# Optimization experiments

Measured on AMD Instinct MI355X. Metric: run time of the kernel, lower is better.

The kernel has to match this reference:

```python
import jax, jax.numpy as jnp
import numpy as np
from jax import lax

T_LOW, T_HIGH = 100.0, 200.0   # init kwargs of Canny
TG22 = 0.4142135623730951      # tan(22.5 deg), cv2's direction quantization constant
MAX_ITERS = 512                # safety cap on hysteresis fixed-point loop


def _shift(a, dy, dx):
    # neighbor value n[y, x] = a[y + dy, x + dx], zero outside
    H, W = a.shape
    p = jnp.pad(a, 1)
    return p[1 + dy:1 + dy + H, 1 + dx:1 + dx + W]


def _canny(x):
    B, C, H, W = x.shape
    # toRGB: ((x+1)/2*255).to(uint8)  (truncation; values are non-negative)
    img = jnp.clip(jnp.floor((x + 1.0) * 0.5 * 255.0), 0.0, 255.0)
    # original reshapes batch into one tall strip (B*H, W, C) before cv2.Canny
    img = img.transpose(0, 2, 3, 1).reshape(B * H, W, C)
    HH = B * H
    p = jnp.pad(img, ((1, 1), (1, 1), (0, 0)), mode='edge')  # replicate border like cv2

    def s(dy, dx):
        return p[1 + dy:1 + dy + HH, 1 + dx:1 + dx + W, :]

    # 3x3 Sobel per channel
    gx = (s(-1, 1) + 2.0 * s(0, 1) + s(1, 1)) - (s(-1, -1) + 2.0 * s(0, -1) + s(1, -1))
    gy = (s(1, -1) + 2.0 * s(1, 0) + s(1, 1)) - (s(-1, -1) + 2.0 * s(-1, 0) + s(-1, 1))
    mag_c = jnp.abs(gx) + jnp.abs(gy)  # L1 magnitude (cv2 default L2gradient=False)
    # multi-channel: take channel with max magnitude per pixel (cv2 behavior)
    idx = jnp.argmax(mag_c, axis=-1, keepdims=True)
    gx = jnp.take_along_axis(gx, idx, -1)[..., 0]
    gy = jnp.take_along_axis(gy, idx, -1)[..., 0]
    mag = jnp.take_along_axis(mag_c, idx, -1)[..., 0]

    # non-maximum suppression with 4 quantized directions
    ax_, ay_ = jnp.abs(gx), jnp.abs(gy)
    is_h = ay_ < TG22 * ax_          # gradient ~horizontal -> compare left/right
    is_v = ay_ * TG22 > ax_          # gradient ~vertical -> compare up/down
    same = (gx * gy) >= 0.0          # diagonal orientation by sign agreement
    n1 = jnp.where(is_h, _shift(mag, 0, -1),
         jnp.where(is_v, _shift(mag, -1, 0),
         jnp.where(same, _shift(mag, -1, -1), _shift(mag, -1, 1))))
    n2 = jnp.where(is_h, _shift(mag, 0, 1),
         jnp.where(is_v, _shift(mag, 1, 0),
         jnp.where(same, _shift(mag, 1, 1), _shift(mag, 1, -1))))
    keep = (mag > n1) & (mag >= n2)

    strong = keep & (mag > T_HIGH)
    weak = keep & (mag > T_LOW)

    # hysteresis: propagate strong labels through 8-connected weak pixels to fixed point
    def dilate(m):
        mf = m.astype(jnp.float32)
        return lax.reduce_window(mf, 0.0, lax.add, (3, 3), (1, 1), 'SAME') > 0.0

    def body(st):
        s0, _, it = st
        grown = (dilate(s0) & weak) | s0
        return grown, jnp.any(grown != s0), it + 1

    def cond(st):
        return st[1] & (st[2] < MAX_ITERS)

    strong, _, _ = lax.while_loop(cond, body, (strong, jnp.array(True), jnp.array(0)))

    edges = strong.reshape(B, H, W).astype(jnp.float32)        # {0,1} == cv2 {0,255}/255
    edges = jnp.broadcast_to(edges[:, None, :, :], (B, 3, H, W))
    return (edges - 0.5) / 0.5                                 # T.Normalize(0.5, 0.5)


def setup_inputs() -> dict:
    key = jax.random.key(0)
    x = jax.random.uniform(key, (16, 3, 512, 512), jnp.float32, -1.0, 1.0)
    return {"x": x}


def reference(x):
    return _canny(x)
```

## Files before the change

kernel.cpp:

```cpp
#include <hip/hip_runtime.h>
#include <stdint.h>

#define HH 8192
#define WW 512
#define WPR 8
#define TG22F 0.4142135623730951f
#define NROUND 8
#define NBLK 32


__device__ __forceinline__ float to_img(float v) {
    float t = floorf((v + 1.0f) * 0.5f * 255.0f);
    return fminf(fmaxf(t, 0.0f), 255.0f);
}

__device__ __forceinline__ int bsel(uint64_t w0, uint64_t w1, int idx) {
    return (idx < 8) ? (int)((w0 >> (idx * 8)) & 255)
                     : (int)((w1 >> ((idx - 8) * 8)) & 255);
}

__device__ __forceinline__ uint64_t runfill(uint64_t s, uint64_t w) {
    uint64_t sw = s & w;
    uint64_t up = ((sw + w) ^ w) & w;
    uint64_t rs = __brevll(sw);
    uint64_t rw = __brevll(w);
    uint64_t dn = __brevll(((rs + rw) ^ rw) & rw);
    return up | dn | sw;
}

__device__ __forceinline__ uint64_t shfl_up64(uint64_t v, int d) {
    int lo = __shfl_up((int)(uint32_t)v, d, 64);
    int hi = __shfl_up((int)(uint32_t)(v >> 32), d, 64);
    return ((uint64_t)(uint32_t)hi << 32) | (uint32_t)lo;
}
__device__ __forceinline__ uint64_t shfl_dn64(uint64_t v, int d) {
    int lo = __shfl_down((int)(uint32_t)v, d, 64);
    int hi = __shfl_down((int)(uint32_t)(v >> 32), d, 64);
    return ((uint64_t)(uint32_t)hi << 32) | (uint32_t)lo;
}

__device__ __forceinline__ uint64_t cload64(const unsigned long long* p) {
    return __hip_atomic_load((const unsigned long long*)p, __ATOMIC_RELAXED,
                             __HIP_MEMORY_SCOPE_AGENT);
}
__device__ __forceinline__ void cstore64(unsigned long long* p, uint64_t v) {
    __hip_atomic_store(p, (unsigned long long)v, __ATOMIC_RELAXED,
                       __HIP_MEMORY_SCOPE_AGENT);
}

__global__ void k_sobel(const float* __restrict__ in, uint16_t* __restrict__ packed) {
    __shared__ uint8_t simg[3 * 34 * 72];
    const int tid = threadIdx.x;
    const int row0 = (blockIdx.x >> 3) << 5;
    const int col0 = (blockIdx.x & 7) << 6;

    for (int i = tid; i < 1632; i += 256) {
        int c = i / 544;
        int rem = i - c * 544;
        int hr = rem >> 4;
        int q = rem & 15;
        int gy = row0 + hr - 1;
        gy = gy < 0 ? 0 : (gy >= HH ? HH - 1 : gy);
        int b = gy >> 9, h = gy & 511;
        const float4 v = *(const float4*)&in[((((b * 3 + c) << 9) + h) << 9) + col0 + (q << 2)];
        uint32_t pk = (uint32_t)(uint8_t)to_img(v.x)
                    | ((uint32_t)(uint8_t)to_img(v.y) << 8)
                    | ((uint32_t)(uint8_t)to_img(v.z) << 16)
                    | ((uint32_t)(uint8_t)to_img(v.w) << 24);
        *(uint32_t*)&simg[(c * 34 + hr) * 72 + 4 + (q << 2)] = pk;
    }
    for (int i = tid; i < 204; i += 256) {
        int c = i / 68;
        int rem = i - c * 68;
        int hr = rem >> 1;
        int side = rem & 1;
        int gy = row0 + hr - 1;
        gy = gy < 0 ? 0 : (gy >= HH ? HH - 1 : gy);
        int gc = side ? col0 + 64 : col0 - 1;
        gc = gc < 0 ? 0 : (gc >= WW ? WW - 1 : gc);
        int b = gy >> 9, h = gy & 511;
        float v = to_img(in[((((b * 3 + c) << 9) + h) << 9) + gc]);
        simg[(c * 34 + hr) * 72 + (side ? 68 : 3)] = (uint8_t)v;
    }
    __syncthreads();

    const int r = tid >> 3;
    const int c8 = (tid & 7) << 3;

    int bestMag[8], bgx[8], bgy[8];
    #pragma unroll
    for (int j = 0; j < 8; ++j) { bestMag[j] = -1; bgx[j] = 0; bgy[j] = 0; }

    #pragma unroll
    for (int c = 0; c < 3; ++c) {
        const uint8_t* base = &simg[(c * 34 + r) * 72 + c8];
        uint64_t w00 = *(const uint64_t*)(base);
        uint64_t w01 = *(const uint64_t*)(base + 8);
        uint64_t w10 = *(const uint64_t*)(base + 72);
        uint64_t w11 = *(const uint64_t*)(base + 80);
        uint64_t w20 = *(const uint64_t*)(base + 144);
        uint64_t w21 = *(const uint64_t*)(base + 152);
        int vs[10], t0[10], t2[10];
        #pragma unroll
        for (int i = 0; i < 10; ++i) {
            int a0 = bsel(w00, w01, 3 + i);
            int a1 = bsel(w10, w11, 3 + i);
            int a2 = bsel(w20, w21, 3 + i);
            vs[i] = a0 + 2 * a1 + a2;
            t0[i] = a0; t2[i] = a2;
        }
        #pragma unroll
        for (int j = 0; j < 8; ++j) {
            int gx = vs[j + 2] - vs[j];
            int gy = (t2[j] + 2 * t2[j + 1] + t2[j + 2]) - (t0[j] + 2 * t0[j + 1] + t0[j + 2]);
            int mg = abs(gx) + abs(gy);
            if (mg > bestMag[j]) { bestMag[j] = mg; bgx[j] = gx; bgy[j] = gy; }
        }
    }

    uint32_t res[4];
    #pragma unroll
    for (int jj = 0; jj < 4; ++jj) {
        uint32_t pair = 0;
        #pragma unroll
        for (int s = 0; s < 2; ++s) {
            int j = jj * 2 + s;
            float axf = (float)abs(bgx[j]);
            float ayf = (float)abs(bgy[j]);
            int dir;
            if (ayf < TG22F * axf)      dir = 0;
            else if (ayf * TG22F > axf) dir = 1;
            else                        dir = (bgx[j] * bgy[j] >= 0) ? 2 : 3;
            uint32_t val = (uint32_t)(bestMag[j] | (dir << 12));
            pair |= val << (s * 16);
        }
        res[jj] = pair;
    }
    int y = row0 + r;
    *(uint4*)&packed[y * WW + col0 + c8] = *(uint4*)res;
}

#define MEXT(lo, hi, idx) ((int)((((idx) < 4 ? ((lo) >> (16 * (idx))) \
                                             : ((hi) >> (16 * ((idx) - 4))))) & 0xFFF))

__global__ void k_nms(const uint16_t* __restrict__ packed,
                      unsigned long long* __restrict__ strongB,
                      unsigned long long* __restrict__ weakB,
                      int* __restrict__ flags) {
    if (blockIdx.x == 0 && threadIdx.x < 16) flags[threadIdx.x] = 0;
    const int lane = threadIdx.x & 63;
    const int w = threadIdx.x >> 6;
    const int y = (blockIdx.x << 2) + w;

    uint4 q = *(const uint4*)&packed[y * WW + (lane << 3)];
    uint64_t oLo = ((uint64_t)q.y << 32) | q.x;
    uint64_t oHi = ((uint64_t)q.w << 32) | q.z;
    uint64_t uLo = 0, uHi = 0, dLo = 0, dHi = 0;
    if (y > 0) {
        uint4 qu = *(const uint4*)&packed[(y - 1) * WW + (lane << 3)];
        uLo = ((uint64_t)qu.y << 32) | qu.x;
        uHi = ((uint64_t)qu.w << 32) | qu.z;
    }
    if (y < HH - 1) {
        uint4 qd = *(const uint4*)&packed[(y + 1) * WW + (lane << 3)];
        dLo = ((uint64_t)qd.y << 32) | qd.x;
        dHi = ((uint64_t)qd.w << 32) | qd.z;
    }

    int oL = __shfl_up((int)((oHi >> 48) & 0xFFF), 1, 64); if (lane == 0) oL = 0;
    int uL = __shfl_up((int)((uHi >> 48) & 0xFFF), 1, 64); if (lane == 0) uL = 0;
    int dL = __shfl_up((int)((dHi >> 48) & 0xFFF), 1, 64); if (lane == 0) dL = 0;
    int oR = __shfl_down((int)(oLo & 0xFFF), 1, 64); if (lane == 63) oR = 0;
    int uR = __shfl_down((int)(uLo & 0xFFF), 1, 64); if (lane == 63) uR = 0;
    int dR = __shfl_down((int)(dLo & 0xFFF), 1, 64); if (lane == 63) dR = 0;

    uint32_t sb = 0, wb = 0;
    #pragma unroll
    for (int i = 0; i < 8; ++i) {
        int raw = (int)(((i < 4 ? (oLo >> (16 * i)) : (oHi >> (16 * (i - 4))))) & 0xFFFF);
        int m = raw & 0xFFF;
        int dir = raw >> 12;
        int Om1 = (i == 0) ? oL : MEXT(oLo, oHi, (i == 0 ? 0 : i - 1));
        int Op1 = (i == 7) ? oR : MEXT(oLo, oHi, (i == 7 ? 7 : i + 1));
        int Ui  = MEXT(uLo, uHi, i);
        int Um1 = (i == 0) ? uL : MEXT(uLo, uHi, (i == 0 ? 0 : i - 1));
        int Up1 = (i == 7) ? uR : MEXT(uLo, uHi, (i == 7 ? 7 : i + 1));
        int Di  = MEXT(dLo, dHi, i);
        int Dm1 = (i == 0) ? dL : MEXT(dLo, dHi, (i == 0 ? 0 : i - 1));
        int Dp1 = (i == 7) ? dR : MEXT(dLo, dHi, (i == 7 ? 7 : i + 1));
        int n1 = (dir == 0) ? Om1 : (dir == 1) ? Ui : (dir == 2) ? Um1 : Up1;
        int n2 = (dir == 0) ? Op1 : (dir == 1) ? Di : (dir == 2) ? Dp1 : Dm1;
        bool keep = (m > n1) && (m >= n2);
        if (keep && m > 200) sb |= 1u << i;
        if (keep && m > 100) wb |= 1u << i;
    }

    const int src = (lane & 7) << 3;
    uint64_t wordS = 0, wordW = 0;
    #pragma unroll
    for (int i = 0; i < 8; ++i) {
        wordS |= (uint64_t)(uint32_t)__shfl((int)sb, src + i, 64) << (i * 8);
        wordW |= (uint64_t)(uint32_t)__shfl((int)wb, src + i, 64) << (i * 8);
    }
    if (lane < 8)       strongB[y * WPR + lane] = wordS;
    else if (lane < 16) weakB[y * WPR + (lane - 8)] = wordW;
}

__global__ void __launch_bounds__(256) k_hyst(
        const unsigned long long* __restrict__ weakB,
        unsigned long long* __restrict__ buf,
        int* __restrict__ flags)
{
    const int lane = threadIdx.x & 63;
    const int wave = (blockIdx.x << 2) + (threadIdx.x >> 6);
    const int base = ((wave << 6) + lane) * WPR;

    uint64_t own[8], wk[8];
    #pragma unroll
    for (int k = 0; k < 8; ++k) { wk[k] = weakB[base + k]; own[k] = buf[base + k]; }

    uint64_t hspu[8], hspd[8];
    #pragma unroll
    for (int k = 0; k < 8; ++k) { hspu[k] = 0; hspd[k] = 0; }

    auto load_halo = [&]() {
        uint64_t h[8];
        if (lane == 0 && wave > 0) {
            #pragma unroll
            for (int k = 0; k < 8; ++k) h[k] = cload64(&buf[base - WPR + k]);
            #pragma unroll
            for (int k = 0; k < 8; ++k) {
                uint64_t a = h[k] | (h[k] << 1) | (h[k] >> 1);
                if (k > 0) a |= h[k - 1] >> 63;
                if (k < 7) a |= h[k + 1] << 63;
                hspu[k] = a;
            }
        }
        if (lane == 63 && wave < 127) {
            #pragma unroll
            for (int k = 0; k < 8; ++k) h[k] = cload64(&buf[base + WPR + k]);
            #pragma unroll
            for (int k = 0; k < 8; ++k) {
                uint64_t a = h[k] | (h[k] << 1) | (h[k] >> 1);
                if (k > 0) a |= h[k - 1] >> 63;
                if (k < 7) a |= h[k + 1] << 63;
                hspd[k] = a;
            }
        }
    };
    load_halo();

    bool grewAny = false;
    for (int r = 0; r < NROUND; ++r) {
        bool grew = false;
        for (;;) {
            uint64_t sp[8];
            #pragma unroll
            for (int k = 0; k < 8; ++k) {
                uint64_t h = own[k] | (own[k] << 1) | (own[k] >> 1);
                if (k > 0) h |= own[k - 1] >> 63;
                if (k < 7) h |= own[k + 1] << 63;
                sp[k] = h;
            }
            uint64_t su[8], sd[8];
            #pragma unroll
            for (int k = 0; k < 8; ++k) {
                su[k] = shfl_up64(sp[k], 1);
                sd[k] = shfl_dn64(sp[k], 1);
            }
            if (lane == 0) {
                #pragma unroll
                for (int k = 0; k < 8; ++k) su[k] = hspu[k];
            }
            if (lane == 63) {
                #pragma unroll
                for (int k = 0; k < 8; ++k) sd[k] = hspd[k];
            }
            uint32_t ch = 0;
            #pragma unroll
            for (int k = 0; k < 8; ++k) {
                uint64_t acc = sp[k] | su[k] | sd[k];
                uint64_t nv = runfill(own[k] | (acc & wk[k]), wk[k]);
                ch |= (uint32_t)(nv != own[k]);
                own[k] = nv;
            }
            if (ch) grew = true;
            if (__ballot(ch ? 1 : 0) == 0ull) break;
        }
        grewAny |= grew;

        if (grew && lane == 0)
            __hip_atomic_store(&flags[r], 1, __ATOMIC_RELAXED, __HIP_MEMORY_SCOPE_AGENT);
        if (lane == 0 || lane == 63) {
            #pragma unroll
            for (int k = 0; k < 8; ++k) cstore64(&buf[base + k], own[k]);
        }
        __syncthreads();
        if (threadIdx.x == 0) {
            __hip_atomic_fetch_add(&flags[8 + r], 1, __ATOMIC_RELAXED, __HIP_MEMORY_SCOPE_AGENT);
            while (__hip_atomic_load(&flags[8 + r], __ATOMIC_RELAXED, __HIP_MEMORY_SCOPE_AGENT) < NBLK)
                __builtin_amdgcn_s_sleep(2);
        }
        __syncthreads();

        if (__hip_atomic_load(&flags[r], __ATOMIC_RELAXED, __HIP_MEMORY_SCOPE_AGENT) == 0)
            break;
        if (r + 1 < NROUND) load_halo();
    }

    if (__ballot(grewAny ? 1 : 0) != 0ull) {
        #pragma unroll
        for (int k = 0; k < 8; ++k) buf[base + k] = own[k];
    }
}

__global__ void k_out(const unsigned long long* __restrict__ result, float* __restrict__ out) {
    int t = blockIdx.x * blockDim.x + threadIdx.x;
    int b = t >> 16;
    int r = t & 65535;
    int h = r >> 7;
    int w = (r & 127) << 2;
    int y = (b << 9) + h;
    unsigned long long word = result[y * WPR + (w >> 6)];
    int sh = w & 63;
    float4 v;
    v.x = ((word >> (sh + 0)) & 1ull) ? 1.0f : -1.0f;
    v.y = ((word >> (sh + 1)) & 1ull) ? 1.0f : -1.0f;
    v.z = ((word >> (sh + 2)) & 1ull) ? 1.0f : -1.0f;
    v.w = ((word >> (sh + 3)) & 1ull) ? 1.0f : -1.0f;
    int base = (b * 3) << 18;
    int off = (h << 9) + w;
    *(float4*)&out[base + off] = v;
    *(float4*)&out[base + 262144 + off] = v;
    *(float4*)&out[base + 524288 + off] = v;
}

extern "C" void kernel_launch(void* const* d_in, const int* in_sizes, int n_in,
                              void* d_out, int out_size, void* d_ws, size_t ws_size,
                              hipStream_t stream) {
    const float* x = (const float*)d_in[0];
    float* out = (float*)d_out;
    char* ws = (char*)d_ws;

    uint16_t* packed          = (uint16_t*)(ws);
    unsigned long long* buf   = (unsigned long long*)(ws + 8388608);
    unsigned long long* weakB = (unsigned long long*)(ws + 8912896);
    int* flags                = (int*)(ws + 9437184);

    k_sobel<<<2048, 256, 0, stream>>>(x, packed);
    k_nms<<<2048, 256, 0, stream>>>(packed, buf, weakB, flags);
    k_hyst<<<NBLK, 256, 0, stream>>>(weakB, buf, flags);
    k_out<<<4096, 256, 0, stream>>>(buf, out);
}
```

Measured before the change: 122.9 us.

## Fuse NMS, hysteresis and output into one persistent kernel with grid barriers

Merges the NMS, hysteresis and output-expansion kernels into a single persistent kernel of 512 blocks. Two software grid barriers built on atomic counters separate the phases, and only the first 32 blocks run the hysteresis loop. Flag clearing moves into the Sobel kernel. The aim is to remove two kernel launches and their gaps, at the cost of idle blocks spinning during hysteresis and relying on all 512 blocks being co-resident.

```diff
diff --git a/kernel.cpp b/kernel.cpp
--- a/kernel.cpp
+++ b/kernel.cpp
@@ -7,6 +7,7 @@
 #define TG22F 0.4142135623730951f
 #define NROUND 8
 #define NBLK 32
+#define TBLK 512
 
 
 __device__ __forceinline__ float to_img(float v) {
@@ -48,11 +49,24 @@
                        __HIP_MEMORY_SCOPE_AGENT);
 }
 
-__global__ void k_sobel(const float* __restrict__ in, uint16_t* __restrict__ packed) {
+__device__ __forceinline__ void gbar(int* flags, int slot, int target) {
+    __syncthreads();
+    if (threadIdx.x == 0) {
+        __hip_atomic_fetch_add(&flags[slot], 1, __ATOMIC_RELAXED, __HIP_MEMORY_SCOPE_AGENT);
+        while (__hip_atomic_load(&flags[slot], __ATOMIC_RELAXED, __HIP_MEMORY_SCOPE_AGENT) < target)
+            __builtin_amdgcn_s_sleep(2);
+    }
+    __syncthreads();
+}
+
+__global__ void k_sobel(const float* __restrict__ in, uint16_t* __restrict__ packed,
+                        int* __restrict__ flags) {
     __shared__ uint8_t simg[3 * 34 * 72];
     const int tid = threadIdx.x;
     const int row0 = (blockIdx.x >> 3) << 5;
     const int col0 = (blockIdx.x & 7) << 6;
+
+    if (blockIdx.x == 0 && tid < 32) flags[tid] = 0;
 
     for (int i = tid; i < 1632; i += 256) {
         int c = i / 544;
@@ -143,15 +157,10 @@
 #define MEXT(lo, hi, idx) ((int)((((idx) < 4 ? ((lo) >> (16 * (idx))) \
                                              : ((hi) >> (16 * ((idx) - 4))))) & 0xFFF))
 
-__global__ void k_nms(const uint16_t* __restrict__ packed,
-                      unsigned long long* __restrict__ strongB,
-                      unsigned long long* __restrict__ weakB,
-                      int* __restrict__ flags) {
-    if (blockIdx.x == 0 && threadIdx.x < 16) flags[threadIdx.x] = 0;
-    const int lane = threadIdx.x & 63;
-    const int w = threadIdx.x >> 6;
-    const int y = (blockIdx.x << 2) + w;
-
+__device__ __forceinline__ void nms_row(int y, int lane,
+        const uint16_t* __restrict__ packed,
+        unsigned long long* __restrict__ strongB,
+        unsigned long long* __restrict__ weakB) {
     uint4 q = *(const uint4*)&packed[y * WW + (lane << 3)];
     uint64_t oLo = ((uint64_t)q.y << 32) | q.x;
     uint64_t oHi = ((uint64_t)q.w << 32) | q.z;
@@ -202,137 +211,159 @@
         wordS |= (uint64_t)(uint32_t)__shfl((int)sb, src + i, 64) << (i * 8);
         wordW |= (uint64_t)(uint32_t)__shfl((int)wb, src + i, 64) << (i * 8);
     }
-    if (lane < 8)       strongB[y * WPR + lane] = wordS;
-    else if (lane < 16) weakB[y * WPR + (lane - 8)] = wordW;
-}
-
-__global__ void __launch_bounds__(256) k_hyst(
-        const unsigned long long* __restrict__ weakB,
+    if (lane < 8)       cstore64(&strongB[y * WPR + lane], wordS);
+    else if (lane < 16) cstore64(&weakB[y * WPR + (lane - 8)], wordW);
+}
+
+__device__ __forceinline__ void out_row(int y, int lane,
+        const unsigned long long* __restrict__ buf, float* __restrict__ out) {
+    const int b = y >> 9, h = y & 511;
+    const int obase = ((b * 3) << 18) + (h << 9);
+    #pragma unroll
+    for (int i = 0; i < 2; ++i) {
+        int idx = lane + (i << 6);
+        uint64_t wv = cload64(&buf[y * WPR + (idx >> 4)]);
+        int x = idx << 2;
+        int sh = x & 63;
+        float4 v;
+        v.x = ((wv >> (sh + 0)) & 1ull) ? 1.0f : -1.0f;
+        v.y = ((wv >> (sh + 1)) & 1ull) ? 1.0f : -1.0f;
+        v.z = ((wv >> (sh + 2)) & 1ull) ? 1.0f : -1.0f;
+        v.w = ((wv >> (sh + 3)) & 1ull) ? 1.0f : -1.0f;
+        *(float4*)&out[obase + x] = v;
+        *(float4*)&out[obase + (1 << 18) + x] = v;
+        *(float4*)&out[obase + (2 << 18) + x] = v;
+    }
+}
+
+__global__ void __launch_bounds__(256) k_nho(
+        const uint16_t* __restrict__ packed,
         unsigned long long* __restrict__ buf,
-        int* __restrict__ flags)
+        unsigned long long* __restrict__ weakB,
+        int* __restrict__ flags,
+        float* __restrict__ out)
 {
     const int lane = threadIdx.x & 63;
-    const int wave = (blockIdx.x << 2) + (threadIdx.x >> 6);
-    const int base = ((wave << 6) + lane) * WPR;
-
-    uint64_t own[8], wk[8];
-    #pragma unroll
-    for (int k = 0; k < 8; ++k) { wk[k] = weakB[base + k]; own[k] = buf[base + k]; }
-
-    uint64_t hspu[8], hspd[8];
-    #pragma unroll
-    for (int k = 0; k < 8; ++k) { hspu[k] = 0; hspd[k] = 0; }
-
-    auto load_halo = [&]() {
-        uint64_t h[8];
-        if (lane == 0 && wave > 0) {
-            #pragma unroll
-            for (int k = 0; k < 8; ++k) h[k] = cload64(&buf[base - WPR + k]);
-            #pragma unroll
-            for (int k = 0; k < 8; ++k) {
-                uint64_t a = h[k] | (h[k] << 1) | (h[k] >> 1);
-                if (k > 0) a |= h[k - 1] >> 63;
-                if (k < 7) a |= h[k + 1] << 63;
-                hspu[k] = a;
-            }
-        }
-        if (lane == 63 && wave < 127) {
-            #pragma unroll
-            for (int k = 0; k < 8; ++k) h[k] = cload64(&buf[base + WPR + k]);
-            #pragma unroll
-            for (int k = 0; k < 8; ++k) {
-                uint64_t a = h[k] | (h[k] << 1) | (h[k] >> 1);
-                if (k > 0) a |= h[k - 1] >> 63;
-                if (k < 7) a |= h[k + 1] << 63;
-                hspd[k] = a;
-            }
-        }
-    };
-    load_halo();
-
-    bool grewAny = false;
-    for (int r = 0; r < NROUND; ++r) {
-        bool grew = false;
-        for (;;) {
-            uint64_t sp[8];
-            #pragma unroll
-            for (int k = 0; k < 8; ++k) {
-                uint64_t h = own[k] | (own[k] << 1) | (own[k] >> 1);
-                if (k > 0) h |= own[k - 1] >> 63;
-                if (k < 7) h |= own[k + 1] << 63;
-                sp[k] = h;
-            }
-            uint64_t su[8], sd[8];
-            #pragma unroll
-            for (int k = 0; k < 8; ++k) {
-                su[k] = shfl_up64(sp[k], 1);
-                sd[k] = shfl_dn64(sp[k], 1);
-            }
-            if (lane == 0) {
-                #pragma unroll
-                for (int k = 0; k < 8; ++k) su[k] = hspu[k];
-            }
-            if (lane == 63) {
-                #pragma unroll
-                for (int k = 0; k < 8; ++k) sd[k] = hspd[k];
-            }
-            uint32_t ch = 0;
-            #pragma unroll
-            for (int k = 0; k < 8; ++k) {
-                uint64_t acc = sp[k] | su[k] | sd[k];
-                uint64_t nv = runfill(own[k] | (acc & wk[k]), wk[k]);
-                ch |= (uint32_t)(nv != own[k]);
-                own[k] = nv;
-            }
-            if (ch) grew = true;
-            if (__ballot(ch ? 1 : 0) == 0ull) break;
-        }
-        grewAny |= grew;
-
-        if (grew && lane == 0)
-            __hip_atomic_store(&flags[r], 1, __ATOMIC_RELAXED, __HIP_MEMORY_SCOPE_AGENT);
-        if (lane == 0 || lane == 63) {
+    const int widx = threadIdx.x >> 6;
+    const int wv = (blockIdx.x << 2) + widx;
+
+    #pragma unroll
+    for (int r = 0; r < 4; ++r)
+        nms_row((wv << 2) + r, lane, packed, buf, weakB);
+
+    gbar(flags, 16, TBLK);
+
+    if (blockIdx.x < NBLK) {
+        const int wave = (blockIdx.x << 2) + widx;
+        const int base = ((wave << 6) + lane) * WPR;
+
+        uint64_t own[8], wk[8];
+        #pragma unroll
+        for (int k = 0; k < 8; ++k) {
+            wk[k]  = cload64(&weakB[base + k]);
+            own[k] = cload64(&buf[base + k]);
+        }
+
+        uint64_t hspu[8], hspd[8];
+        #pragma unroll
+        for (int k = 0; k < 8; ++k) { hspu[k] = 0; hspd[k] = 0; }
+
+        auto load_halo = [&]() {
+            uint64_t h[8];
+            if (lane == 0 && wave > 0) {
+                #pragma unroll
+                for (int k = 0; k < 8; ++k) h[k] = cload64(&buf[base - WPR + k]);
+                #pragma unroll
+                for (int k = 0; k < 8; ++k) {
+                    uint64_t a = h[k] | (h[k] << 1) | (h[k] >> 1);
+                    if (k > 0) a |= h[k - 1] >> 63;
+                    if (k < 7) a |= h[k + 1] << 63;
+                    hspu[k] = a;
+                }
+            }
+            if (lane == 63 && wave < 127) {
+                #pragma unroll
+                for (int k = 0; k < 8; ++k) h[k] = cload64(&buf[base + WPR + k]);
+                #pragma unroll
+                for (int k = 0; k < 8; ++k) {
+                    uint64_t a = h[k] | (h[k] << 1) | (h[k] >> 1);
+                    if (k > 0) a |= h[k - 1] >> 63;
+                    if (k < 7) a |= h[k + 1] << 63;
+                    hspd[k] = a;
+                }
+            }
+        };
+        load_halo();
+
+        bool grewAny = false;
+        for (int r = 0; r < NROUND; ++r) {
+            bool grew = false;
+            for (;;) {
+                uint64_t sp[8];
+                #pragma unroll
+                for (int k = 0; k < 8; ++k) {
+                    uint64_t h = own[k] | (own[k] << 1) | (own[k] >> 1);
+                    if (k > 0) h |= own[k - 1] >> 63;
+                    if (k < 7) h |= own[k + 1] << 63;
+                    sp[k] = h;
+                }
+                uint64_t su[8], sd[8];
+                #pragma unroll
+                for (int k = 0; k < 8; ++k) {
+                    su[k] = shfl_up64(sp[k], 1);
+                    sd[k] = shfl_dn64(sp[k], 1);
+                }
+                if (lane == 0) {
+                    #pragma unroll
+                    for (int k = 0; k < 8; ++k) su[k] = hspu[k];
+                }
+                if (lane == 63) {
+                    #pragma unroll
+                    for (int k = 0; k < 8; ++k) sd[k] = hspd[k];
+                }
+                uint32_t ch = 0;
+                #pragma unroll
+                for (int k = 0; k < 8; ++k) {
+                    uint64_t acc = sp[k] | su[k] | sd[k];
+                    uint64_t nv = runfill(own[k] | (acc & wk[k]), wk[k]);
+                    ch |= (uint32_t)(nv != own[k]);
+                    own[k] = nv;
+                }
+                if (ch) grew = true;
+                if (__ballot(ch ? 1 : 0) == 0ull) break;
+            }
+            grewAny |= grew;
+
+            if (grew && lane == 0)
+                __hip_atomic_store(&flags[r], 1, __ATOMIC_RELAXED, __HIP_MEMORY_SCOPE_AGENT);
+            if (lane == 0 || lane == 63) {
+                #pragma unroll
+                for (int k = 0; k < 8; ++k) cstore64(&buf[base + k], own[k]);
+            }
+            __syncthreads();
+            if (threadIdx.x == 0) {
+                __hip_atomic_fetch_add(&flags[8 + r], 1, __ATOMIC_RELAXED, __HIP_MEMORY_SCOPE_AGENT);
+                while (__hip_atomic_load(&flags[8 + r], __ATOMIC_RELAXED, __HIP_MEMORY_SCOPE_AGENT) < NBLK)
+                    __builtin_amdgcn_s_sleep(2);
+            }
+            __syncthreads();
+
+            if (__hip_atomic_load(&flags[r], __ATOMIC_RELAXED, __HIP_MEMORY_SCOPE_AGENT) == 0)
+                break;
+            if (r + 1 < NROUND) load_halo();
+        }
+
+        if (__ballot(grewAny ? 1 : 0) != 0ull) {
             #pragma unroll
             for (int k = 0; k < 8; ++k) cstore64(&buf[base + k], own[k]);
         }
-        __syncthreads();
-        if (threadIdx.x == 0) {
-            __hip_atomic_fetch_add(&flags[8 + r], 1, __ATOMIC_RELAXED, __HIP_MEMORY_SCOPE_AGENT);
-            while (__hip_atomic_load(&flags[8 + r], __ATOMIC_RELAXED, __HIP_MEMORY_SCOPE_AGENT) < NBLK)
-                __builtin_amdgcn_s_sleep(2);
-        }
-        __syncthreads();
-
-        if (__hip_atomic_load(&flags[r], __ATOMIC_RELAXED, __HIP_MEMORY_SCOPE_AGENT) == 0)
-            break;
-        if (r + 1 < NROUND) load_halo();
-    }
-
-    if (__ballot(grewAny ? 1 : 0) != 0ull) {
-        #pragma unroll
-        for (int k = 0; k < 8; ++k) buf[base + k] = own[k];
-    }
-}
-
-__global__ void k_out(const unsigned long long* __restrict__ result, float* __restrict__ out) {
-    int t = blockIdx.x * blockDim.x + threadIdx.x;
-    int b = t >> 16;
-    int r = t & 65535;
-    int h = r >> 7;
-    int w = (r & 127) << 2;
-    int y = (b << 9) + h;
-    unsigned long long word = result[y * WPR + (w >> 6)];
-    int sh = w & 63;
-    float4 v;
-    v.x = ((word >> (sh + 0)) & 1ull) ? 1.0f : -1.0f;
-    v.y = ((word >> (sh + 1)) & 1ull) ? 1.0f : -1.0f;
-    v.z = ((word >> (sh + 2)) & 1ull) ? 1.0f : -1.0f;
-    v.w = ((word >> (sh + 3)) & 1ull) ? 1.0f : -1.0f;
-    int base = (b * 3) << 18;
-    int off = (h << 9) + w;
-    *(float4*)&out[base + off] = v;
-    *(float4*)&out[base + 262144 + off] = v;
-    *(float4*)&out[base + 524288 + off] = v;
+    }
+
+    gbar(flags, 17, TBLK);
+
+    #pragma unroll
+    for (int r = 0; r < 4; ++r)
+        out_row((wv << 2) + r, lane, buf, out);
 }
 
 extern "C" void kernel_launch(void* const* d_in, const int* in_sizes, int n_in,
@@ -347,8 +378,6 @@
     unsigned long long* weakB = (unsigned long long*)(ws + 8912896);
     int* flags                = (int*)(ws + 9437184);
 
-    k_sobel<<<2048, 256, 0, stream>>>(x, packed);
-    k_nms<<<2048, 256, 0, stream>>>(packed, buf, weakB, flags);
-    k_hyst<<<NBLK, 256, 0, stream>>>(weakB, buf, flags);
-    k_out<<<4096, 256, 0, stream>>>(buf, out);
-}
+    k_sobel<<<2048, 256, 0, stream>>>(x, packed, flags);
+    k_nho<<<TBLK, 256, 0, stream>>>(packed, buf, weakB, flags, out);
+}
```

Result: slower. 150.6 us (+22.5%).

## Replace shared-memory tiled Sobel with per-wave row loads and lane shuffles

Applied to the files above, without the earlier changes.

The Sobel kernel no longer stages a 32x64 tile plus halo into shared memory. Each wavefront now handles one full image row, loading the three neighbouring rows directly from global memory and exchanging left/right halo pixels with lane shuffles. This removes the LDS staging, the __syncthreads barrier and the byte-extraction logic. In exchange every input row is read three times from global memory (relying on cache), and the launch geometry must match the new one-row-per-wave mapping.

```diff
diff --git a/kernel.cpp b/kernel.cpp
--- a/kernel.cpp
+++ b/kernel.cpp
@@ -12,11 +12,6 @@
 __device__ __forceinline__ float to_img(float v) {
     float t = floorf((v + 1.0f) * 0.5f * 255.0f);
     return fminf(fmaxf(t, 0.0f), 255.0f);
-}
-
-__device__ __forceinline__ int bsel(uint64_t w0, uint64_t w1, int idx) {
-    return (idx < 8) ? (int)((w0 >> (idx * 8)) & 255)
-                     : (int)((w1 >> ((idx - 8) * 8)) & 255);
 }
 
 __device__ __forceinline__ uint64_t runfill(uint64_t s, uint64_t w) {
@@ -48,44 +43,31 @@
                        __HIP_MEMORY_SCOPE_AGENT);
 }
 
+__device__ __forceinline__ void load_row10(const float* __restrict__ in,
+                                           int row, int c, int lane, int a[10]) {
+    const float* p = &in[(size_t)((((row >> 9) * 3 + c) << 9) + (row & 511)) << 9];
+    const int x0 = lane << 3;
+    float4 v0 = *(const float4*)&p[x0];
+    float4 v1 = *(const float4*)&p[x0 + 4];
+    a[1] = (int)(uint8_t)to_img(v0.x);
+    a[2] = (int)(uint8_t)to_img(v0.y);
+    a[3] = (int)(uint8_t)to_img(v0.z);
+    a[4] = (int)(uint8_t)to_img(v0.w);
+    a[5] = (int)(uint8_t)to_img(v1.x);
+    a[6] = (int)(uint8_t)to_img(v1.y);
+    a[7] = (int)(uint8_t)to_img(v1.z);
+    a[8] = (int)(uint8_t)to_img(v1.w);
+    int l = __shfl_up(a[8], 1, 64);
+    a[0] = (lane == 0) ? a[1] : l;
+    int r = __shfl_down(a[1], 1, 64);
+    a[9] = (lane == 63) ? a[8] : r;
+}
+
 __global__ void k_sobel(const float* __restrict__ in, uint16_t* __restrict__ packed) {
-    __shared__ uint8_t simg[3 * 34 * 72];
-    const int tid = threadIdx.x;
-    const int row0 = (blockIdx.x >> 3) << 5;
-    const int col0 = (blockIdx.x & 7) << 6;
-
-    for (int i = tid; i < 1632; i += 256) {
-        int c = i / 544;
-        int rem = i - c * 544;
-        int hr = rem >> 4;
-        int q = rem & 15;
-        int gy = row0 + hr - 1;
-        gy = gy < 0 ? 0 : (gy >= HH ? HH - 1 : gy);
-        int b = gy >> 9, h = gy & 511;
-        const float4 v = *(const float4*)&in[((((b * 3 + c) << 9) + h) << 9) + col0 + (q << 2)];
-        uint32_t pk = (uint32_t)(uint8_t)to_img(v.x)
-                    | ((uint32_t)(uint8_t)to_img(v.y) << 8)
-                    | ((uint32_t)(uint8_t)to_img(v.z) << 16)
-                    | ((uint32_t)(uint8_t)to_img(v.w) << 24);
-        *(uint32_t*)&simg[(c * 34 + hr) * 72 + 4 + (q << 2)] = pk;
-    }
-    for (int i = tid; i < 204; i += 256) {
-        int c = i / 68;
-        int rem = i - c * 68;
-        int hr = rem >> 1;
-        int side = rem & 1;
-        int gy = row0 + hr - 1;
-        gy = gy < 0 ? 0 : (gy >= HH ? HH - 1 : gy);
-        int gc = side ? col0 + 64 : col0 - 1;
-        gc = gc < 0 ? 0 : (gc >= WW ? WW - 1 : gc);
-        int b = gy >> 9, h = gy & 511;
-        float v = to_img(in[((((b * 3 + c) << 9) + h) << 9) + gc]);
-        simg[(c * 34 + hr) * 72 + (side ? 68 : 3)] = (uint8_t)v;
-    }
-    __syncthreads();
-
-    const int r = tid >> 3;
-    const int c8 = (tid & 7) << 3;
+    const int lane = threadIdx.x & 63;
+    const int y  = (blockIdx.x << 2) + (threadIdx.x >> 6);
+    const int ym = (y > 0) ? y - 1 : 0;
+    const int yp = (y < HH - 1) ? y + 1 : HH - 1;
 
     int bestMag[8], bgx[8], bgy[8];
     #pragma unroll
@@ -93,26 +75,17 @@
 
     #pragma unroll
     for (int c = 0; c < 3; ++c) {
-        const uint8_t* base = &simg[(c * 34 + r) * 72 + c8];
-        uint64_t w00 = *(const uint64_t*)(base);
-        uint64_t w01 = *(const uint64_t*)(base + 8);
-        uint64_t w10 = *(const uint64_t*)(base + 72);
-        uint64_t w11 = *(const uint64_t*)(base + 80);
-        uint64_t w20 = *(const uint64_t*)(base + 144);
-        uint64_t w21 = *(const uint64_t*)(base + 152);
-        int vs[10], t0[10], t2[10];
+        int a0[10], a1[10], a2[10];
+        load_row10(in, ym, c, lane, a0);
+        load_row10(in, y,  c, lane, a1);
+        load_row10(in, yp, c, lane, a2);
+        int vs[10];
         #pragma unroll
-        for (int i = 0; i < 10; ++i) {
-            int a0 = bsel(w00, w01, 3 + i);
-            int a1 = bsel(w10, w11, 3 + i);
-            int a2 = bsel(w20, w21, 3 + i);
-            vs[i] = a0 + 2 * a1 + a2;
-            t0[i] = a0; t2[i] = a2;
-        }
+        for (int i = 0; i < 10; ++i) vs[i] = a0[i] + 2 * a1[i] + a2[i];
         #pragma unroll
         for (int j = 0; j < 8; ++j) {
             int gx = vs[j + 2] - vs[j];
-            int gy = (t2[j] + 2 * t2[j + 1] + t2[j + 2]) - (t0[j] + 2 * t0[j + 1] + t0[j + 2]);
+            int gy = (a2[j] + 2 * a2[j + 1] + a2[j + 2]) - (a0[j] + 2 * a0[j + 1] + a0[j + 2]);
             int mg = abs(gx) + abs(gy);
             if (mg > bestMag[j]) { bestMag[j] = mg; bgx[j] = gx; bgy[j] = gy; }
         }
@@ -136,8 +109,7 @@
         }
         res[jj] = pair;
     }
-    int y = row0 + r;
-    *(uint4*)&packed[y * WW + col0 + c8] = *(uint4*)res;
+    *(uint4*)&packed[y * WW + (lane << 3)] = *(uint4*)res;
 }
 
 #define MEXT(lo, hi, idx) ((int)((((idx) < 4 ? ((lo) >> (16 * (idx))) \
```

Result: faster. 119.5 us (-2.8%).
